# Optimization experiments

Hardware: AMD Instinct MI355X
Metric: run time of the kernel (lower is better)

Reference implementation:

```python
import jax, jax.numpy as jnp
import numpy as np

B, T, S, D, H, DK, DV, DFF = 2, 2048, 2048, 1024, 16, 64, 64, 4096
EPS = 1e-5


def layer_norm(x, g, b):
    m = jnp.mean(x, axis=-1, keepdims=True)
    v = jnp.var(x, axis=-1, keepdims=True)
    return (x - m) * jax.lax.rsqrt(v + EPS) * g + b


def mha(q_in, k_in, v_in, Wq, bq, Wk, bk, Wv, bv, Wo, bo, mask):
    # q_in: [B, Lq, D]; k_in/v_in: [B, Lk, D]
    Q = (q_in @ Wq + bq).reshape(q_in.shape[0], -1, H, DK).transpose(0, 2, 1, 3)  # [B,H,Lq,dk]
    K = (k_in @ Wk + bk).reshape(k_in.shape[0], -1, H, DK).transpose(0, 2, 1, 3)
    V = (v_in @ Wv + bv).reshape(v_in.shape[0], -1, H, DV).transpose(0, 2, 1, 3)
    scores = jnp.einsum('bhqd,bhkd->bhqk', Q, K) / jnp.float32(np.sqrt(DK))
    scores = jnp.where(mask == 0, jnp.float32(-1e9), scores)
    attn = jax.nn.softmax(scores, axis=-1)
    out = jnp.einsum('bhqk,bhkd->bhqd', attn, V)
    out = out.transpose(0, 2, 1, 3).reshape(q_in.shape[0], -1, H * DV)
    return out @ Wo + bo


def setup_inputs() -> dict:
    key = jax.random.key(0)
    ks = jax.random.split(key, 16)
    s = 0.02
    inp = {
        'x': jax.random.normal(ks[0], (B, T, D), jnp.float32),
        'encoder_output': jax.random.normal(ks[1], (B, S, D), jnp.float32),
        'lookahead_mask': jnp.tril(jnp.ones((T, T), jnp.int32))[None, None],  # [1,1,T,T]
        'padding_mask': jnp.ones((1, 1, 1, S), jnp.int32),
        # self-attention params
        'sa_Wq': jax.random.normal(ks[2], (D, H * DK), jnp.float32) * s,
        'sa_bq': jnp.zeros((H * DK,), jnp.float32),
        'sa_Wk': jax.random.normal(ks[3], (D, H * DK), jnp.float32) * s,
        'sa_bk': jnp.zeros((H * DK,), jnp.float32),
        'sa_Wv': jax.random.normal(ks[4], (D, H * DV), jnp.float32) * s,
        'sa_bv': jnp.zeros((H * DV,), jnp.float32),
        'sa_Wo': jax.random.normal(ks[5], (H * DV, D), jnp.float32) * s,
        'sa_bo': jnp.zeros((D,), jnp.float32),
        # cross-attention params
        'ca_Wq': jax.random.normal(ks[6], (D, H * DK), jnp.float32) * s,
        'ca_bq': jnp.zeros((H * DK,), jnp.float32),
        'ca_Wk': jax.random.normal(ks[7], (D, H * DK), jnp.float32) * s,
        'ca_bk': jnp.zeros((H * DK,), jnp.float32),
        'ca_Wv': jax.random.normal(ks[8], (D, H * DV), jnp.float32) * s,
        'ca_bv': jnp.zeros((H * DV,), jnp.float32),
        'ca_Wo': jax.random.normal(ks[9], (H * DV, D), jnp.float32) * s,
        'ca_bo': jnp.zeros((D,), jnp.float32),
        # feed-forward params
        'ff_W1': jax.random.normal(ks[10], (D, DFF), jnp.float32) * s,
        'ff_b1': jnp.zeros((DFF,), jnp.float32),
        'ff_W2': jax.random.normal(ks[11], (DFF, D), jnp.float32) * s,
        'ff_b2': jnp.zeros((D,), jnp.float32),
        # layer norms
        'ln1_g': jnp.ones((D,), jnp.float32), 'ln1_b': jnp.zeros((D,), jnp.float32),
        'ln2_g': jnp.ones((D,), jnp.float32), 'ln2_b': jnp.zeros((D,), jnp.float32),
        'ln3_g': jnp.ones((D,), jnp.float32), 'ln3_b': jnp.zeros((D,), jnp.float32),
    }
    return inp


def reference(x, encoder_output, lookahead_mask, padding_mask,
              sa_Wq, sa_bq, sa_Wk, sa_bk, sa_Wv, sa_bv, sa_Wo, sa_bo,
              ca_Wq, ca_bq, ca_Wk, ca_bk, ca_Wv, ca_bv, ca_Wo, ca_bo,
              ff_W1, ff_b1, ff_W2, ff_b2,
              ln1_g, ln1_b, ln2_g, ln2_b, ln3_g, ln3_b):
    attn1 = mha(x, x, x, sa_Wq, sa_bq, sa_Wk, sa_bk, sa_Wv, sa_bv, sa_Wo, sa_bo, lookahead_mask)
    addnorm1 = layer_norm(x + attn1, ln1_g, ln1_b)
    attn2 = mha(addnorm1, encoder_output, encoder_output,
                ca_Wq, ca_bq, ca_Wk, ca_bk, ca_Wv, ca_bv, ca_Wo, ca_bo, padding_mask)
    addnorm2 = layer_norm(addnorm1 + attn2, ln2_g, ln2_b)
    ff = jax.nn.relu(addnorm2 @ ff_W1 + ff_b1) @ ff_W2 + ff_b2
    return layer_norm(addnorm2 + ff, ln3_g, ln3_b)
```

## Files before the change

### kernel.cpp

```cpp
#include <hip/hip_runtime.h>

typedef unsigned short u16;
typedef unsigned int   u32;
typedef __attribute__((ext_vector_type(8)))  __bf16 bf16x8;
typedef __attribute__((ext_vector_type(4)))  float  f32x4;
typedef __attribute__((ext_vector_type(16))) float  f32x16;
typedef __attribute__((ext_vector_type(4)))  unsigned short u16x4;

#define DEV static __device__ __forceinline__

#define SC 0.1803368801111243f

DEV u16 cvt_bf16(float f){
  u32 u = __builtin_bit_cast(u32, f);
  u32 r = (u + 0x7FFFu + ((u >> 16) & 1u)) >> 16;
  return (u16)r;
}
DEV float bf2f(u16 v){ return __builtin_bit_cast(float, (u32)v << 16); }

typedef __attribute__((address_space(1))) void* as1p;
typedef __attribute__((address_space(3))) void* as3p;

DEV void gld16(void* lds, const void* g){
  __builtin_amdgcn_global_load_lds((as1p)g, (as3p)lds, 16, 0, 0);
}

DEV f32x4 mfma16(bf16x8 a, bf16x8 b, f32x4 c){
  return __builtin_amdgcn_mfma_f32_16x16x32_bf16(a, b, c, 0, 0, 0);
}
DEV f32x16 mfma32(bf16x8 a, bf16x8 b, f32x16 c){
  return __builtin_amdgcn_mfma_f32_32x32x16_bf16(a, b, c, 0, 0, 0);
}

DEV bf16x8 ld8(const u16* p){ return *(const bf16x8*)p; }

DEV float vexp2(float x){
  float y; asm("v_exp_f32 %0, %1" : "=v"(y) : "v"(x)); return y;
}

DEV u32 cvtpk(float lo, float hi){
  u32 r; asm("v_cvt_pk_bf16_f32 %0, %1, %2" : "=v"(r) : "v"(lo), "v"(hi)); return r;
}
DEV void perm32swap(u32 &a, u32 &b){
  asm("v_permlane32_swap_b32 %0, %1" : "+v"(a), "+v"(b));
}
DEV bf16x8 frag4(u32 w0,u32 w1,u32 w2,u32 w3){
  union{ u32 w[4]; bf16x8 f; } u; u.w[0]=w0; u.w[1]=w1; u.w[2]=w2; u.w[3]=w3; return u.f;
}

DEV int swz64(int row, int blk){ return row*64 + ((blk ^ (row & 7)) << 3); }
DEV int swz32(int row, int blk){ return row*32 + ((blk ^ (row & 3)) << 3); }

__global__ __launch_bounds__(256) void castk2(const float* __restrict__ in0,
                                              u16* __restrict__ out0,
                                              const float* __restrict__ in1,
                                              u16* __restrict__ out1){
  const float* in = blockIdx.y ? in1 : in0;
  u16*        out = blockIdx.y ? out1 : out0;
  int i = blockIdx.x*256 + threadIdx.x;
  f32x4 v = *(const f32x4*)(in + (size_t)i*4);
  u16x4 o;
  #pragma unroll
  for(int j=0;j<4;j++) o[j] = cvt_bf16(v[j]);
  *(u16x4*)(out + (size_t)i*4) = o;
}

__global__ __launch_bounds__(256) void smallfuse(
    const float* __restrict__ sabq, const float* __restrict__ sabk,
    const float* __restrict__ sabv, const float* __restrict__ cabk,
    const float* __restrict__ cabv, const float* __restrict__ cabq,
    const int* __restrict__ pm,
    float* __restrict__ bqkv, float* __restrict__ bkvc,
    float* __restrict__ biasg, float* __restrict__ bqc){
  int i = blockIdx.x*256 + threadIdx.x;
  if(i < 1024)       bqkv[i] = sabq[i]*SC;
  else if(i < 2048)  bqkv[i] = sabk[i-1024];
  else if(i < 3072)  bqkv[i] = sabv[i-2048];
  else if(i < 4096)  bkvc[i-3072] = cabk[i-3072];
  else if(i < 5120)  bkvc[i-3072] = cabv[i-4096];
  else if(i < 7168)  biasg[i-5120] = pm[i-5120] ? 0.f : -1e9f;
  else if(i < 8192)  bqc[i-7168] = cabq[i-7168]*SC;
}

DEV void wcast_body(const float* __restrict__ W, u16* __restrict__ Wt,
                    int K, int N, int bx, int by, int tid, float scale){
  __shared__ u16 tile[64][66];
  const int k0 = bx*64, n0 = by*64;
  const int lr = tid >> 4, c4 = (tid & 15)*4;
  #pragma unroll
  for(int p=0;p<4;p++){
    const int r = lr + p*16;
    f32x4 v = *(const f32x4*)&W[(size_t)(k0+r)*N + n0 + c4];
    #pragma unroll
    for(int j=0;j<4;j++) tile[r][c4+j] = cvt_bf16(v[j]*scale);
  }
  __syncthreads();
  #pragma unroll
  for(int p=0;p<4;p++){
    const int n = lr + p*16;
    u16x4 u;
    #pragma unroll
    for(int j=0;j<4;j++) u[j] = tile[c4+j][n];
    *(u16x4*)&Wt[(size_t)(n0+n)*K + k0 + c4] = u;
  }
}

__global__ __launch_bounds__(256) void wcast_t(const float* __restrict__ W,
                                               u16* __restrict__ Wt, int K, int N){
  wcast_body(W, Wt, K, N, blockIdx.x, blockIdx.y, threadIdx.x, 1.f);
}

__global__ __launch_bounds__(256) void wcast8(
    const float* s0, const float* s1, const float* s2, const float* s3,
    const float* s4, const float* s5, const float* s6, const float* s7,
    u16* d0, u16* d1, u16* d2, u16* d3, u16* d4, u16* d5, u16* d6, u16* d7){
  const float* W; u16* Wt;
  switch(blockIdx.z){
    case 0: W=s0; Wt=d0; break;  case 1: W=s1; Wt=d1; break;
    case 2: W=s2; Wt=d2; break;  case 3: W=s3; Wt=d3; break;
    case 4: W=s4; Wt=d4; break;  case 5: W=s5; Wt=d5; break;
    case 6: W=s6; Wt=d6; break;  default: W=s7; Wt=d7; break;
  }
  const float scale = (blockIdx.z==0 || blockIdx.z==4) ? SC : 1.f;
  wcast_body(W, Wt, 1024, 1024, blockIdx.x, blockIdx.y, threadIdx.x, scale);
}

__global__ __launch_bounds__(256) void vtrans(const u16* __restrict__ V,
                                              u16* __restrict__ Vt, int L, int ld){
  __shared__ u16 tile[64][66];
  const int t0 = blockIdx.x*64;
  const int h = blockIdx.y, b = blockIdx.z;
  const int lr = threadIdx.x >> 4, c4 = (threadIdx.x & 15)*4;
  #pragma unroll
  for(int p=0;p<4;p++){
    const int r = lr + p*16;
    u16x4 v = *(const u16x4*)&V[(size_t)(b*L + t0 + r)*ld + h*64 + c4];
    #pragma unroll
    for(int j=0;j<4;j++) tile[r][c4+j] = v[j];
  }
  __syncthreads();
  #pragma unroll
  for(int p=0;p<4;p++){
    const int d = lr + p*16;
    u16x4 u;
    #pragma unroll
    for(int j=0;j<4;j++) u[j] = tile[c4+j][d];
    *(u16x4*)&Vt[((size_t)((b*16 + h)*64 + d))*L + t0 + c4] = u;
  }
}

template<int OMODE, int BN, int SPLITK>
__global__ __launch_bounds__(256, BN==128 ? 3 : 4) void gemm_bt(
    const u16* __restrict__ A, const u16* __restrict__ Bt,
    const float* __restrict__ bias, void* __restrict__ Cout0, void* __restrict__ Cout1,
    int N, int K)
{
  __shared__ __align__(16) u16 As[2][128*32];
  __shared__ __align__(16) u16 Bs[2][BN*32];
  constexpr int NJ = BN/32;
  const int tid = threadIdx.x, wave = tid>>6, lane = tid&63;
  const int fr = lane&15, fg = lane>>4;
  const int bm = blockIdx.x*128, bn = blockIdx.y*BN;
  const int part = (SPLITK>1) ? blockIdx.z : 0;
  const int Kp = K / SPLITK;
  const int kbase = part * Kp;
  const int wm = (wave>>1)*64, wn = (wave&1)*(BN/2);
  const f32x4 z4 = {0.f,0.f,0.f,0.f};
  f32x4 acc[4][NJ];
  #pragma unroll
  for(int i=0;i<4;i++)
    #pragma unroll
    for(int j=0;j<NJ;j++) acc[i][j] = z4;

  const int srA = wave*32 + (lane>>2);
  const int cl_l = (lane&3)*8;
  const int cl_g = ((lane&3) ^ ((lane>>2)&3))*8;
  const int srB = (BN==128) ? srA : (wave*16 + (lane>>2));
  const u16* gA = A  + (size_t)(bm + srA)*K + kbase + cl_g;
  const u16* gB = Bt + (size_t)(bn + srB)*K + kbase + cl_g;

  auto stage = [&](int p, int ko){
    u16* lA = &As[p][srA*32 + cl_l];
    u16* lB = &Bs[p][srB*32 + cl_l];
    gld16(lA,     gA + ko);
    gld16(lA+512, gA + ko + (size_t)16*K);
    gld16(lB,     gB + ko);
    if(BN==128) gld16(lB+512, gB + ko + (size_t)16*K);
  };

  const int nk = Kp >> 5;
  stage(0, 0);
  __syncthreads();
  for(int kt=0; kt<nk; ++kt){
    const int cur = kt & 1;
    if(kt+1 < nk) stage(cur^1, (kt+1)*32);
    bf16x8 af[4], bfv[NJ];
    #pragma unroll
    for(int i=0;i<4;i++) af[i] = ld8(&As[cur][swz32(wm + i*16 + fr, fg)]);
    #pragma unroll
    for(int j=0;j<NJ;j++) bfv[j] = ld8(&Bs[cur][swz32(wn + j*16 + fr, fg)]);
    __builtin_amdgcn_s_setprio(1);
    #pragma unroll
    for(int i=0;i<4;i++)
      #pragma unroll
      for(int j=0;j<NJ;j++)
        acc[i][j] = mfma16(af[i], bfv[j], acc[i][j]);
    __builtin_amdgcn_s_setprio(0);
    __syncthreads();
  }

  void* Cout = (part==0) ? Cout0 : Cout1;
  const int r0 = bm + wm + fg*4;
  const int c0 = bn + wn + fr;
  #pragma unroll
  for(int j=0;j<NJ;j++){
    const int col = c0 + j*16;
    const float bv = (part==0) ? bias[col] : 0.f;
    #pragma unroll
    for(int i=0;i<4;i++){
      #pragma unroll
      for(int r=0;r<4;r++){
        const float v = acc[i][j][r] + bv;
        const size_t idx = (size_t)(r0 + i*16 + r)*N + col;
        if(OMODE==0)      ((float*)Cout)[idx] = v;
        else if(OMODE==1) ((u16*)Cout)[idx]   = cvt_bf16(v);
        else              ((u16*)Cout)[idx]   = cvt_bf16(fmaxf(v, 0.f));
      }
    }
  }
}

template<bool CAUSAL, int NPART>
__global__ __launch_bounds__(256,4) void attn3(
    const u16* __restrict__ Qg, int ldq, const u16* __restrict__ Kg, int ldk,
    const u16* __restrict__ Vt, const float* __restrict__ biasg,
    u16* __restrict__ O0, u16* __restrict__ O1,
    u16* __restrict__ O2, u16* __restrict__ O3,
    float* __restrict__ Ll, int Lk)
{
  __shared__ __align__(16) u16 Ks[2][64*64];
  __shared__ __align__(16) u16 Vs[2][64*64];
  constexpr int P2 = NPART*16;
  const int tid = threadIdx.x, wave = tid>>6, lane = tid&63;
  const int l31 = lane&31, hi = lane>>5;
  const int bid = blockIdx.x;
  const int g    = (bid&7)*4 + ((bid>>3)/P2);
  const int rp   = (bid>>3)%P2;
  const int part = rp&(NPART-1), qb = rp/NPART;
  const int h = g&15, b = g>>4;
  const int qi = CAUSAL ? ((qb&1) ? (15-(qb>>1)) : (qb>>1)) : qb;
  const int q0 = qi*128;
  const int qw = q0 + wave*32;
  const int qrow = qw + l31;

  bf16x8 qf[4];
  {
    const u16* Qp = Qg + (size_t)(b*2048 + qrow)*ldq + h*64;
    #pragma unroll
    for(int c=0;c<4;c++) qf[c] = ld8(Qp + c*16 + hi*8);
  }

  f32x16 o0, o1;
  #pragma unroll
  for(int r=0;r<16;r++){ o0[r]=0.f; o1[r]=0.f; }
  float lsum = 0.f;

  const int srow = wave*16 + (lane>>3);
  const int cl_l = (lane&7)*8;
  const int cl_g = ((lane&7) ^ ((lane>>3)&7))*8;
  const u16* Kp = Kg + (size_t)(b*2048 + srow)*ldk + h*64 + cl_g;
  const u16* Vp = Vt + ((size_t)((b*16 + h)*64 + srow))*Lk + cl_g;

  auto stage = [&](int p, int kv0){
    u16* lK = &Ks[p][srow*64 + cl_l];
    u16* lV = &Vs[p][srow*64 + cl_l];
    gld16(lK,     Kp + (size_t)kv0*ldk);
    gld16(lK+512, Kp + (size_t)(kv0+8)*ldk);
    gld16(lV,     Vp + kv0);
    gld16(lV+512, Vp + kv0 + 8*(size_t)Lk);
  };

  const int T  = CAUSAL ? (2*qi+2) : (Lk>>6);
  const int t0 = part*T/NPART, t1 = (part+1)*T/NPART;

  stage(0, t0*64);
  __syncthreads();
  for(int kt=t0; kt<t1; ++kt){
    const int cur = (kt-t0)&1;
    const int kv0 = kt*64;
    if(kt+1 < t1) stage(cur^1, (kt+1)*64);

    if(!CAUSAL || kv0 <= qw+31){
      f32x16 s0, s1;
      #pragma unroll
      for(int r=0;r<16;r++){ s0[r]=0.f; s1[r]=0.f; }
      __builtin_amdgcn_s_setprio(1);
      #pragma unroll
      for(int c=0;c<4;c++){
        bf16x8 k0 = ld8(&Ks[cur][swz64(l31,      2*c+hi)]);
        bf16x8 k1 = ld8(&Ks[cur][swz64(32 + l31, 2*c+hi)]);
        s0 = mfma32(k0, qf[c], s0);
        s1 = mfma32(k1, qf[c], s1);
      }
      __builtin_amdgcn_s_setprio(0);

      float p[32];
      #pragma unroll
      for(int r=0;r<16;r++){ p[r]=s0[r]; p[16+r]=s1[r]; }

      if(CAUSAL){
        if(kv0 + 63 > qw){
          #pragma unroll
          for(int n=0;n<2;n++)
            #pragma unroll
            for(int r=0;r<16;r++){
              const int kc = kv0 + 32*n + (r&3) + 8*(r>>2) + 4*hi;
              if(kc > qrow) p[16*n+r] = -1e9f;
            }
        }
      } else {
        #pragma unroll
        for(int n=0;n<2;n++)
          #pragma unroll
          for(int cq=0;cq<4;cq++){
            f32x4 bv = *(const f32x4*)&biasg[kv0 + 32*n + 8*cq + 4*hi];
            #pragma unroll
            for(int i=0;i<4;i++) p[16*n+4*cq+i] += bv[i];
          }
      }

      float rs0=0.f, rs1=0.f, rs2=0.f, rs3=0.f;
      #pragma unroll
      for(int r=0;r<8;r++){
        p[r]    = vexp2(p[r]);    rs0 += p[r];
        p[8+r]  = vexp2(p[8+r]);  rs1 += p[8+r];
        p[16+r] = vexp2(p[16+r]); rs2 += p[16+r];
        p[24+r] = vexp2(p[24+r]); rs3 += p[24+r];
      }
      float rs = (rs0+rs1) + (rs2+rs3);
      rs += __shfl_xor(rs, 32);
      lsum += rs;

      u32 pw[16];
      #pragma unroll
      for(int n=0;n<2;n++)
        #pragma unroll
        for(int cp=0;cp<2;cp++){
          const int base = 16*n + 8*cp, cc = 2*n + cp;
          u32 a1 = cvtpk(p[base+0], p[base+1]);
          u32 a2 = cvtpk(p[base+2], p[base+3]);
          u32 b1 = cvtpk(p[base+4], p[base+5]);
          u32 b2 = cvtpk(p[base+6], p[base+7]);
          perm32swap(a1, b1);
          perm32swap(a2, b2);
          pw[4*cc+0]=a1; pw[4*cc+1]=a2; pw[4*cc+2]=b1; pw[4*cc+3]=b2;
        }

      __builtin_amdgcn_s_setprio(1);
      #pragma unroll
      for(int cc=0;cc<4;cc++){
        bf16x8 pf = frag4(pw[4*cc], pw[4*cc+1], pw[4*cc+2], pw[4*cc+3]);
        bf16x8 v0 = ld8(&Vs[cur][swz64(l31,      2*cc+hi)]);
        bf16x8 v1 = ld8(&Vs[cur][swz64(32 + l31, 2*cc+hi)]);
        o0 = mfma32(pf, v0, o0);
        o1 = mfma32(pf, v1, o1);
      }
      __builtin_amdgcn_s_setprio(0);
    }
    __syncthreads();
  }

  u16* Obase = (part==0) ? O0 : (part==1) ? O1 : (part==2) ? O2 : O3;
  u16* Op = Obase + (size_t)(b*2048 + qw)*1024 + h*64;
  #pragma unroll
  for(int r=0;r<16;r++){
    const int qidx = (r&3) + 8*(r>>2) + 4*hi;
    Op[(size_t)qidx*1024 + l31]      = cvt_bf16(o0[r]);
    Op[(size_t)qidx*1024 + 32 + l31] = cvt_bf16(o1[r]);
  }
  if(hi==0){
    const int mi = part*65536 + h*4096 + (b*2048 + qw + l31);
    Ll[mi] = lsum;
  }
}

template<int NP>
__global__ __launch_bounds__(256) void att_combine(
    const u16* __restrict__ O0, const u16* __restrict__ O1,
    const u16* __restrict__ O2, const u16* __restrict__ O3,
    const float* __restrict__ Ll, u16* __restrict__ Ob)
{
  const int row = blockIdx.x, tid = threadIdx.x;
  const int h = tid>>4;
  const int mi = h*4096 + row;
  float denom = 0.f;
  #pragma unroll
  for(int p=0;p<NP;p++) denom += Ll[p*65536 + mi];
  const float inv = 1.f/denom;
  const size_t base = (size_t)row*1024 + tid*4;
  f32x4 acc = {0.f,0.f,0.f,0.f};
  #pragma unroll
  for(int p=0;p<NP;p++){
    const u16* Op = (p==0) ? O0 : (p==1) ? O1 : (p==2) ? O2 : O3;
    u16x4 a = *(const u16x4*)(Op + base);
    #pragma unroll
    for(int j=0;j<4;j++) acc[j] += bf2f(a[j]);
  }
  u16x4 o;
  #pragma unroll
  for(int j=0;j<4;j++) o[j] = cvt_bf16(acc[j]*inv);
  *(u16x4*)(Ob + base) = o;
}

__global__ __launch_bounds__(256) void add_ln3(const float* __restrict__ X,
                        const float* __restrict__ D1, const float* __restrict__ D2,
                        const float* __restrict__ gam, const float* __restrict__ bet,
                        float* __restrict__ outf, u16* __restrict__ outb){
  __shared__ float red[8];
  const int tid = threadIdx.x, wave = tid>>6, lane = tid&63;
  const size_t base = ((size_t)blockIdx.x << 10) + tid*4;
  f32x4 xv = *(const f32x4*)(X + base);
  f32x4 d1 = *(const f32x4*)(D1 + base);
  f32x4 d2 = *(const f32x4*)(D2 + base);
  f32x4 v;
  #pragma unroll
  for(int j=0;j<4;j++) v[j] = xv[j] + d1[j] + d2[j];
  float s = v[0]+v[1]+v[2]+v[3];
  float q = v[0]*v[0]+v[1]*v[1]+v[2]*v[2]+v[3]*v[3];
  #pragma unroll
  for(int off=1;off<64;off<<=1){ s += __shfl_xor(s,off); q += __shfl_xor(q,off); }
  if(lane==0){ red[wave]=s; red[4+wave]=q; }
  __syncthreads();
  s = red[0]+red[1]+red[2]+red[3];
  q = red[4]+red[5]+red[6]+red[7];
  const float mean = s*(1.f/1024.f);
  const float var  = q*(1.f/1024.f) - mean*mean;
  const float rr = rsqrtf(var + 1e-5f);
  const int c = tid*4;
  f32x4 y;
  #pragma unroll
  for(int j=0;j<4;j++) y[j] = (v[j]-mean)*rr*gam[c+j] + bet[c+j];
  *(f32x4*)(outf + base) = y;
  if(outb){
    u16x4 ob;
    #pragma unroll
    for(int j=0;j<4;j++) ob[j] = cvt_bf16(y[j]);
    *(u16x4*)(outb + base) = ob;
  }
}

extern "C" void kernel_launch(void* const* d_in, const int* in_sizes, int n_in,
                              void* d_out, int out_size, void* d_ws, size_t ws_size,
                              hipStream_t stream)
{
  (void)in_sizes; (void)n_in; (void)out_size; (void)ws_size;
  const float* x    = (const float*)d_in[0];
  const float* enc  = (const float*)d_in[1];
  const int*   pmask= (const int*)d_in[3];
  const float* saWq = (const float*)d_in[4];  const float* sabq = (const float*)d_in[5];
  const float* saWk = (const float*)d_in[6];  const float* sabk = (const float*)d_in[7];
  const float* saWv = (const float*)d_in[8];  const float* sabv = (const float*)d_in[9];
  const float* saWo = (const float*)d_in[10]; const float* sabo = (const float*)d_in[11];
  const float* caWq = (const float*)d_in[12]; const float* cabq = (const float*)d_in[13];
  const float* caWk = (const float*)d_in[14]; const float* cabk = (const float*)d_in[15];
  const float* caWv = (const float*)d_in[16]; const float* cabv = (const float*)d_in[17];
  const float* caWo = (const float*)d_in[18]; const float* cabo = (const float*)d_in[19];
  const float* fW1  = (const float*)d_in[20]; const float* fb1  = (const float*)d_in[21];
  const float* fW2  = (const float*)d_in[22]; const float* fb2  = (const float*)d_in[23];
  const float* l1g  = (const float*)d_in[24]; const float* l1b  = (const float*)d_in[25];
  const float* l2g  = (const float*)d_in[26]; const float* l2b  = (const float*)d_in[27];
  const float* l3g  = (const float*)d_in[28]; const float* l3b  = (const float*)d_in[29];

  char* wsp = (char*)d_ws;
  size_t off = 0;
  auto take = [&](size_t bytes)->void*{ void* p = wsp + off; off += (bytes + 255) & ~(size_t)255; return p; };
  u16* slotA  = (u16*)take(8388608);
  u16* Encb   = (u16*)take(8388608);
  u16* WqkvT  = (u16*)take(6291456);
  u16* cWqT   = (u16*)take(2097152);
  u16* cWkvT  = (u16*)take(4194304);
  u16* WoT    = (u16*)take(2097152);
  u16* cWoT   = (u16*)take(2097152);
  u16* W1T    = (u16*)take(8388608);
  u16* W2T    = (u16*)take(8388608);
  float* bqkv = (float*)take(16384);
  float* bkvc = (float*)take(16384);
  float* biasg= (float*)take(16384);
  float* bqc  = (float*)take(16384);
  u16* slotB  = (u16*)take(25165824);
  u16* Vtb    = (u16*)take(8388608);
  u16* Ob     = (u16*)take(8388608);
  u16* an1b   = (u16*)take(8388608);
  float* projf= (float*)take(16777216);
  float* an1f = (float*)take(16777216);
  float* an2f = (float*)take(16777216);
  char* ffhb  = (char*)take(33554432);
  u16* Xbf = slotA;  u16* Qcb = slotA;  u16* an2b = slotA;
  u16* QKVb = slotB; u16* KVc = slotB;
  u16* ffh   = (u16*)ffhb;
  u16* S0 = (u16*)projf;  u16* S1 = S0 + 4194304;
  u16* S2 = (u16*)an1f;   u16* S3 = S2 + 4194304;
  u16* C0 = (u16*)ffhb;   u16* C1 = C0 + 4194304;
  float* ffp0 = (float*)ffhb;
  float* Llb = (float*)an1b;

  castk2<<<dim3(4096,2),256,0,stream>>>(x, Xbf, enc, Encb);
  wcast8<<<dim3(16,16,8),256,0,stream>>>(
      saWq, saWk, saWv, saWo, caWq, caWk, caWv, caWo,
      WqkvT, WqkvT + 1024*1024, WqkvT + 2*1024*1024, WoT,
      cWqT, cWkvT, cWkvT + 1024*1024, cWoT);
  wcast_t<<<dim3(16,64),256,0,stream>>>(fW1, W1T, 1024, 4096);
  wcast_t<<<dim3(64,16),256,0,stream>>>(fW2, W2T, 4096, 1024);
  smallfuse<<<32,256,0,stream>>>(sabq, sabk, sabv, cabk, cabv, cabq, pmask,
                                 bqkv, bkvc, biasg, bqc);

  gemm_bt<1,128,1><<<dim3(32,24),256,0,stream>>>(Xbf, WqkvT, bqkv, QKVb, nullptr, 3072, 1024);
  vtrans<<<dim3(32,16,2),256,0,stream>>>(QKVb + 2048, Vtb, 2048, 3072);
  attn3<true,4><<<2048,256,0,stream>>>(QKVb, 3072, QKVb + 1024, 3072, Vtb, nullptr,
                                       S0, S1, S2, S3, Llb, 2048);
  att_combine<4><<<4096,256,0,stream>>>(S0, S1, S2, S3, Llb, Ob);
  gemm_bt<0,128,2><<<dim3(32,8,2),256,0,stream>>>(Ob, WoT, sabo, projf, an2f, 1024, 1024);
  add_ln3<<<4096,256,0,stream>>>(x, projf, an2f, l1g, l1b, an1f, an1b);

  gemm_bt<1,64,1><<<dim3(32,16),256,0,stream>>>(an1b, cWqT, bqc, Qcb, nullptr, 1024, 1024);
  gemm_bt<1,128,1><<<dim3(32,16),256,0,stream>>>(Encb, cWkvT, bkvc, KVc, nullptr, 2048, 1024);
  vtrans<<<dim3(32,16,2),256,0,stream>>>(KVc + 1024, Vtb, 2048, 2048);
  attn3<false,2><<<1024,256,0,stream>>>(Qcb, 1024, KVc, 2048, Vtb, biasg,
                                        C0, C1, nullptr, nullptr, Llb, 2048);
  att_combine<2><<<4096,256,0,stream>>>(C0, C1, nullptr, nullptr, Llb, Ob);
  gemm_bt<0,128,2><<<dim3(32,8,2),256,0,stream>>>(Ob, cWoT, cabo, projf, ffp0, 1024, 1024);
  add_ln3<<<4096,256,0,stream>>>(an1f, projf, ffp0, l2g, l2b, an2f, an2b);

  gemm_bt<2,128,1><<<dim3(32,32),256,0,stream>>>(an2b, W1T, fb1, ffh, nullptr, 4096, 1024);
  gemm_bt<0,128,2><<<dim3(32,8,2),256,0,stream>>>(ffh, W2T, fb2, projf, an1f, 1024, 4096);
  add_ln3<<<4096,256,0,stream>>>(an2f, projf, an1f, l3g, l3b, (float*)d_out, nullptr);
}
```

Measured before the change: 401.5 us.

## Triple-buffer GEMM LDS pipeline and store split-K partials as bf16

The GEMM main loop moves from double to triple buffering. Loads are issued two K-steps ahead, and each step waits with explicit vmcnt counts plus a single barrier instead of two __syncthreads. Separately, the split-K partial outputs of the output-projection and FF2 GEMMs are written as bf16 and read back as bf16 in add_ln3, which halves that intermediate traffic. The costs are more LDS per block, which may lower occupancy, and some precision lost on the partial sums before the residual add.

```diff
diff --git a/kernel.cpp b/kernel.cpp
--- a/kernel.cpp
+++ b/kernel.cpp
@@ -155,9 +155,10 @@
     const float* __restrict__ bias, void* __restrict__ Cout0, void* __restrict__ Cout1,
     int N, int K)
 {
-  __shared__ __align__(16) u16 As[2][128*32];
-  __shared__ __align__(16) u16 Bs[2][BN*32];
+  __shared__ __align__(16) u16 As[3][128*32];
+  __shared__ __align__(16) u16 Bs[3][BN*32];
   constexpr int NJ = BN/32;
+  constexpr int LOADS = (BN==128) ? 4 : 3;
   const int tid = threadIdx.x, wave = tid>>6, lane = tid&63;
   const int fr = lane&15, fg = lane>>4;
   const int bm = blockIdx.x*128, bn = blockIdx.y*BN;
@@ -190,10 +191,21 @@
 
   const int nk = Kp >> 5;
   stage(0, 0);
-  __syncthreads();
+  if(nk > 1) stage(1, 32);
+  int cur = 0;
   for(int kt=0; kt<nk; ++kt){
-    const int cur = kt & 1;
-    if(kt+1 < nk) stage(cur^1, (kt+1)*32);
+    if(kt+1 < nk){
+      if constexpr (LOADS==4) asm volatile("s_waitcnt vmcnt(4)" ::: "memory");
+      else                    asm volatile("s_waitcnt vmcnt(3)" ::: "memory");
+    } else {
+      asm volatile("s_waitcnt vmcnt(0)" ::: "memory");
+    }
+    __builtin_amdgcn_s_barrier();
+    asm volatile("" ::: "memory");
+    if(kt+2 < nk){
+      int nb = cur+2; if(nb>=3) nb-=3;
+      stage(nb, (kt+2)*32);
+    }
     bf16x8 af[4], bfv[NJ];
     #pragma unroll
     for(int i=0;i<4;i++) af[i] = ld8(&As[cur][swz32(wm + i*16 + fr, fg)]);
@@ -206,7 +218,7 @@
       for(int j=0;j<NJ;j++)
         acc[i][j] = mfma16(af[i], bfv[j], acc[i][j]);
     __builtin_amdgcn_s_setprio(0);
-    __syncthreads();
+    cur = (cur==2) ? 0 : cur+1;
   }
 
   void* Cout = (part==0) ? Cout0 : Cout1;
@@ -413,18 +425,18 @@
 }
 
 __global__ __launch_bounds__(256) void add_ln3(const float* __restrict__ X,
-                        const float* __restrict__ D1, const float* __restrict__ D2,
+                        const u16* __restrict__ D1, const u16* __restrict__ D2,
                         const float* __restrict__ gam, const float* __restrict__ bet,
                         float* __restrict__ outf, u16* __restrict__ outb){
   __shared__ float red[8];
   const int tid = threadIdx.x, wave = tid>>6, lane = tid&63;
   const size_t base = ((size_t)blockIdx.x << 10) + tid*4;
   f32x4 xv = *(const f32x4*)(X + base);
-  f32x4 d1 = *(const f32x4*)(D1 + base);
-  f32x4 d2 = *(const f32x4*)(D2 + base);
+  u16x4 d1 = *(const u16x4*)(D1 + base);
+  u16x4 d2 = *(const u16x4*)(D2 + base);
   f32x4 v;
   #pragma unroll
-  for(int j=0;j<4;j++) v[j] = xv[j] + d1[j] + d2[j];
+  for(int j=0;j<4;j++) v[j] = xv[j] + bf2f(d1[j]) + bf2f(d2[j]);
   float s = v[0]+v[1]+v[2]+v[3];
   float q = v[0]*v[0]+v[1]*v[1]+v[2]*v[2]+v[3]*v[3];
   #pragma unroll
@@ -501,7 +513,10 @@
   u16* S0 = (u16*)projf;  u16* S1 = S0 + 4194304;
   u16* S2 = (u16*)an1f;   u16* S3 = S2 + 4194304;
   u16* C0 = (u16*)ffhb;   u16* C1 = C0 + 4194304;
-  float* ffp0 = (float*)ffhb;
+  u16* P0 = (u16*)projf;
+  u16* PWo = (u16*)an2f;
+  u16* PcWo= (u16*)ffhb;
+  u16* PFF = (u16*)an1f;
   float* Llb = (float*)an1b;
 
   castk2<<<dim3(4096,2),256,0,stream>>>(x, Xbf, enc, Encb);
@@ -519,8 +534,8 @@
   attn3<true,4><<<2048,256,0,stream>>>(QKVb, 3072, QKVb + 1024, 3072, Vtb, nullptr,
                                        S0, S1, S2, S3, Llb, 2048);
   att_combine<4><<<4096,256,0,stream>>>(S0, S1, S2, S3, Llb, Ob);
-  gemm_bt<0,128,2><<<dim3(32,8,2),256,0,stream>>>(Ob, WoT, sabo, projf, an2f, 1024, 1024);
-  add_ln3<<<4096,256,0,stream>>>(x, projf, an2f, l1g, l1b, an1f, an1b);
+  gemm_bt<1,128,2><<<dim3(32,8,2),256,0,stream>>>(Ob, WoT, sabo, P0, PWo, 1024, 1024);
+  add_ln3<<<4096,256,0,stream>>>(x, P0, PWo, l1g, l1b, an1f, an1b);
 
   gemm_bt<1,64,1><<<dim3(32,16),256,0,stream>>>(an1b, cWqT, bqc, Qcb, nullptr, 1024, 1024);
   gemm_bt<1,128,1><<<dim3(32,16),256,0,stream>>>(Encb, cWkvT, bkvc, KVc, nullptr, 2048, 1024);
@@ -528,10 +543,10 @@
   attn3<false,2><<<1024,256,0,stream>>>(Qcb, 1024, KVc, 2048, Vtb, biasg,
                                         C0, C1, nullptr, nullptr, Llb, 2048);
   att_combine<2><<<4096,256,0,stream>>>(C0, C1, nullptr, nullptr, Llb, Ob);
-  gemm_bt<0,128,2><<<dim3(32,8,2),256,0,stream>>>(Ob, cWoT, cabo, projf, ffp0, 1024, 1024);
-  add_ln3<<<4096,256,0,stream>>>(an1f, projf, ffp0, l2g, l2b, an2f, an2b);
+  gemm_bt<1,128,2><<<dim3(32,8,2),256,0,stream>>>(Ob, cWoT, cabo, P0, PcWo, 1024, 1024);
+  add_ln3<<<4096,256,0,stream>>>(an1f, P0, PcWo, l2g, l2b, an2f, an2b);
 
   gemm_bt<2,128,1><<<dim3(32,32),256,0,stream>>>(an2b, W1T, fb1, ffh, nullptr, 4096, 1024);
-  gemm_bt<0,128,2><<<dim3(32,8,2),256,0,stream>>>(ffh, W2T, fb2, projf, an1f, 1024, 4096);
-  add_ln3<<<4096,256,0,stream>>>(an2f, projf, an1f, l3g, l3b, (float*)d_out, nullptr);
-}
+  gemm_bt<1,128,2><<<dim3(32,8,2),256,0,stream>>>(ffh, W2T, fb2, P0, PFF, 1024, 4096);
+  add_ln3<<<4096,256,0,stream>>>(an2f, P0, PFF, l3g, l3b, (float*)d_out, nullptr);
+}
```

Result: no change. 406.0 us (+1.1%).
